# Kernel optimization log

Hardware: AMD Instinct MI355X
Metric: run time of the kernel (lower is better)

## Reference

```python
import jax, jax.numpy as jnp
import numpy as np

ALPHA, BETA, GAMMA = 1.0, 0.5, 0.3
EPS = 1e-08


def setup_inputs() -> dict:
    key = jax.random.key(0)
    k1, k2, k3, k4, k5 = jax.random.split(key, 5)
    B, C, F = 32, 256, 2048
    return {
        "mag_hat": jax.random.normal(k1, (B, C, F), dtype=jnp.float32),
        "phase_hat": jax.random.normal(k2, (B, C, F), dtype=jnp.float32),
        "mag_target": jax.random.normal(k3, (B, C, F), dtype=jnp.float32),
        "phase_target": jax.random.normal(k4, (B, C, F), dtype=jnp.float32),
        "pci_target": jax.random.uniform(k5, (B, C, C), dtype=jnp.float32),
    }


def _pci(phase):
    # phase: (B, C, F). Naive form is mean_f cos/sin(phi_i - phi_j) over a
    # (B,C,C,F) broadcast; rewrite with cos(a-b)=ca*cb+sa*sb and
    # sin(a-b)=sa*cb-ca*sb as two batched GEMMs on (C,F) matrices.
    c = jnp.cos(phase)
    s = jnp.sin(phase)
    inv_f = 1.0 / phase.shape[-1]
    real = (jnp.einsum('bif,bjf->bij', c, c) + jnp.einsum('bif,bjf->bij', s, s)) * inv_f
    imag = (jnp.einsum('bif,bjf->bij', s, c) - jnp.einsum('bif,bjf->bij', c, s)) * inv_f
    return jnp.sqrt(real * real + imag * imag + EPS)


def reference(mag_hat, phase_hat, mag_target, phase_target, pci_target):
    mag_loss = jnp.mean((mag_hat - mag_target) ** 2)
    phase_loss = jnp.mean(1.0 - jnp.cos(phase_hat - phase_target))
    pci_hat = _pci(phase_hat)
    coh_loss = jnp.mean((pci_hat - pci_target) ** 2)
    total = ALPHA * mag_loss + BETA * phase_loss + GAMMA * coh_loss
    return (total, mag_loss, phase_loss, coh_loss)
```

## Files before the change

kernel.cpp:

```cpp
#include <hip/hip_runtime.h>
#include <hip/hip_bf16.h>

#define ALPHA_ 1.0f
#define BETA_  0.5f
#define GAMMA_ 0.3f
#define EPS_   1e-8f

typedef unsigned short u16;
typedef unsigned int u32;

constexpr int B_ = 32, C_ = 256, F_ = 2048;
constexpr int NTOT = B_ * C_ * F_;
constexpr int NCC  = B_ * C_ * C_;
constexpr int NPOS = 10;
constexpr int KSPL = 4;
constexpr int NBLK = B_ * NPOS * KSPL;
constexpr int NRED = B_ * NPOS * 64 * 64;

__constant__ int TI_[NPOS] = {0, 1, 2, 3, 0, 0, 0, 1, 1, 2};
__constant__ int TJ_[NPOS] = {0, 1, 2, 3, 1, 2, 3, 2, 3, 3};

typedef __bf16 bf16x8 __attribute__((ext_vector_type(8)));
typedef float  f32x4  __attribute__((ext_vector_type(4)));

__device__ __forceinline__ u32 f2bf(float x) {
    unsigned u = __float_as_uint(x);
    u += 0x7fffu + ((u >> 16) & 1u);
    return (u >> 16);
}

__device__ __forceinline__ void ew_body(
    float4 p0, float4 p1, float4 q0, float4 q1,
    float4 a0, float4 a1, float4 b0, float4 b1,
    float& msum, float& psum)
{
    float pv[8] = {p0.x, p0.y, p0.z, p0.w, p1.x, p1.y, p1.z, p1.w};
    float qv[8] = {q0.x, q0.y, q0.z, q0.w, q1.x, q1.y, q1.z, q1.w};
    float av[8] = {a0.x, a0.y, a0.z, a0.w, a1.x, a1.y, a1.z, a1.w};
    float bv[8] = {b0.x, b0.y, b0.z, b0.w, b1.x, b1.y, b1.z, b1.w};
    #pragma unroll
    for (int j = 0; j < 8; j++) {
        float dm = av[j] - bv[j];
        msum += dm * dm;
        psum += 1.f - __cosf(pv[j] - qv[j]);
    }
}

__global__ void __launch_bounds__(256, 4)
ew_kernel(const float4* __restrict__ mh, const float4* __restrict__ ph,
          const float4* __restrict__ mt, const float4* __restrict__ pt,
          float* __restrict__ accum)
{
    __shared__ float sm[4], sp[4];
    const int tid = blockIdx.x * 256 + threadIdx.x;
    constexpr int STR = 1024 * 256;
    float msum = 0.f, psum = 0.f;

    float4 P0[8], P1[8], Q0[8], Q1[8], A0[8], A1[8], B0[8], B1[8];

#define EWLOAD(i) { int g2 = 2 * (tid + (i) * STR);            \
    P0[i] = ph[g2]; P1[i] = ph[g2 + 1];                         \
    Q0[i] = pt[g2]; Q1[i] = pt[g2 + 1];                         \
    A0[i] = mh[g2]; A1[i] = mh[g2 + 1];                         \
    B0[i] = mt[g2]; B1[i] = mt[g2 + 1]; }

    EWLOAD(0);
    #pragma unroll
    for (int i = 0; i < 7; ++i) {
        EWLOAD(i + 1);
        __builtin_amdgcn_sched_barrier(0);
        ew_body(P0[i], P1[i], Q0[i], Q1[i], A0[i], A1[i], B0[i], B1[i], msum, psum);
    }
    ew_body(P0[7], P1[7], Q0[7], Q1[7], A0[7], A1[7], B0[7], B1[7], msum, psum);
#undef EWLOAD

    #pragma unroll
    for (int o = 32; o > 0; o >>= 1) {
        msum += __shfl_down(msum, o, 64);
        psum += __shfl_down(psum, o, 64);
    }
    int lane = threadIdx.x & 63, wv = threadIdx.x >> 6;
    if (lane == 0) { sm[wv] = msum; sp[wv] = psum; }
    __syncthreads();
    if (threadIdx.x == 0) {
        atomicAdd(&accum[0], sm[0] + sm[1] + sm[2] + sm[3]);
        atomicAdd(&accum[1], sp[0] + sp[1] + sp[2] + sp[3]);
    }
}

__device__ __forceinline__ void stage8(float4 a, float4 b, char* base, int pc) {
    float v[8] = {a.x, a.y, a.z, a.w, b.x, b.y, b.z, b.w};
    u32 cu[8], su[8];
    #pragma unroll
    for (int j = 0; j < 8; j++) {
        float s, c;
        __sincosf(v[j], &s, &c);
        cu[j] = f2bf(c);
        su[j] = f2bf(s);
    }
    *(int4*)(base + pc) = make_int4(
        (int)(cu[0] | (cu[1] << 16)), (int)(cu[2] | (cu[3] << 16)),
        (int)(cu[4] | (cu[5] << 16)), (int)(cu[6] | (cu[7] << 16)));
    *(int4*)(base + (pc ^ 128)) = make_int4(
        (int)(su[0] | (su[1] << 16)), (int)(su[2] | (su[3] << 16)),
        (int)(su[4] | (su[5] << 16)), (int)(su[6] | (su[7] << 16)));
}

__global__ void __launch_bounds__(256)
pci_kernel(const float* __restrict__ ph, float* __restrict__ slabs)
{
    __shared__ char lds[32768];
    char* la = lds;
    char* lb = lds + 16384;

    const int bid = blockIdx.x;
    const int l   = (bid & 7) * (NBLK / 8) + (bid >> 3);
    const int h   = l & 3;
    const int t4  = l >> 2;
    const int pos = t4 % NPOS;
    const int y   = t4 / NPOS;
    const int i0 = TI_[pos] * 64, j0 = TJ_[pos] * 64;
    const bool diag = (i0 == j0);
    char* lbp = diag ? la : lb;

    const int t    = threadIdx.x;
    const int lane = t & 63, w = t >> 6;
    const int wrow = (w >> 1) * 32, wcol = (w & 1) * 32;
    const int m = lane & 15, q = lane >> 4;

    const int row0 = t >> 3, oct = t & 7;
    const int row1 = row0 + 32;
    const float* gA0 = ph + ((size_t)(y * 256 + i0 + row0) * 2048 + h * 512 + oct * 8);
    const float* gA1 = ph + ((size_t)(y * 256 + i0 + row1) * 2048 + h * 512 + oct * 8);
    const float* gB0 = ph + ((size_t)(y * 256 + j0 + row0) * 2048 + h * 512 + oct * 8);
    const float* gB1 = ph + ((size_t)(y * 256 + j0 + row1) * 2048 + h * 512 + oct * 8);
    char* dA0 = la + row0 * 256;  const int pc0 = (oct ^ (row0 & 15)) * 16;
    char* dA1 = la + row1 * 256;  const int pc1 = (oct ^ (row1 & 15)) * 16;
    char* dB0 = lb + row0 * 256;
    char* dB1 = lb + row1 * 256;

    f32x4 zero = {0.f, 0.f, 0.f, 0.f};
    f32x4 accR[2][2], accSC[2][2], accCS[2][2];
    #pragma unroll
    for (int a = 0; a < 2; a++)
        #pragma unroll
        for (int c = 0; c < 2; c++) {
            accR[a][c] = zero; accSC[a][c] = zero; accCS[a][c] = zero;
        }

    for (int it = 0; it < 8; ++it) {
        __syncthreads();
        float4 a0 = *(const float4*)gA0, a1 = *(const float4*)(gA0 + 4);
        float4 a2 = *(const float4*)gA1, a3 = *(const float4*)(gA1 + 4);
        float4 b0, b1, b2, b3;
        if (!diag) {
            b0 = *(const float4*)gB0; b1 = *(const float4*)(gB0 + 4);
            b2 = *(const float4*)gB1; b3 = *(const float4*)(gB1 + 4);
        }
        gA0 += 64; gA1 += 64; gB0 += 64; gB1 += 64;
        stage8(a0, a1, dA0, pc0);
        stage8(a2, a3, dA1, pc1);
        if (!diag) {
            stage8(b0, b1, dB0, pc0);
            stage8(b2, b3, dB1, pc1);
        }
        __syncthreads();

        #pragma unroll
        for (int s = 0; s < 2; ++s) {
            bf16x8 fac[2], fas[2], fbc[2], fbs[2];
            #pragma unroll
            for (int a = 0; a < 2; a++) {
                const char* base = la + (wrow + a * 16 + m) * 256;
                int pc = ((4 * s + q) ^ m) * 16;
                fac[a] = *(const bf16x8*)(base + pc);
                fas[a] = *(const bf16x8*)(base + (pc ^ 128));
            }
            #pragma unroll
            for (int c = 0; c < 2; c++) {
                const char* base = lbp + (wcol + c * 16 + m) * 256;
                int pc = ((4 * s + q) ^ m) * 16;
                fbc[c] = *(const bf16x8*)(base + pc);
                fbs[c] = *(const bf16x8*)(base + (pc ^ 128));
            }
            #pragma unroll
            for (int a = 0; a < 2; a++)
                #pragma unroll
                for (int c = 0; c < 2; c++) {
                    accR[a][c]  = __builtin_amdgcn_mfma_f32_16x16x32_bf16(fac[a], fbc[c], accR[a][c], 0, 0, 0);
                    accR[a][c]  = __builtin_amdgcn_mfma_f32_16x16x32_bf16(fas[a], fbs[c], accR[a][c], 0, 0, 0);
                    accSC[a][c] = __builtin_amdgcn_mfma_f32_16x16x32_bf16(fas[a], fbc[c], accSC[a][c], 0, 0, 0);
                    accCS[a][c] = __builtin_amdgcn_mfma_f32_16x16x32_bf16(fac[a], fbs[c], accCS[a][c], 0, 0, 0);
                }
        }
    }

    float* sl = slabs + (size_t)h * ((size_t)NRED * 2)
                      + (size_t)(y * NPOS + pos) * 8192;
    #pragma unroll
    for (int a = 0; a < 2; a++)
        #pragma unroll
        for (int c = 0; c < 2; c++) {
            int ii = wrow + a * 16 + q * 4;
            int jj = wcol + c * 16 + m;
            #pragma unroll
            for (int r = 0; r < 4; r++) {
                int idx = (ii + r) * 64 + jj;
                float2 v = make_float2(accR[a][c][r], accSC[a][c][r] - accCS[a][c][r]);
                *(float2*)(sl + (size_t)idx * 2) = v;
            }
        }
}

__global__ void __launch_bounds__(256)
coh_kernel(const float* __restrict__ slabs, const float* __restrict__ tgt,
           float* __restrict__ accum)
{
    __shared__ float sred[4];
    const int tid  = blockIdx.x * 256 + threadIdx.x;
    const int e0   = tid * 8;
    const int tile = e0 >> 12;
    const int y    = tile / NPOS;
    const int pos  = tile % NPOS;
    const int ii   = (e0 & 4095) >> 6;
    const int jj0  = e0 & 63;
    const int ig   = TI_[pos] * 64 + ii;
    const int jg   = TJ_[pos] * 64 + jj0;
    const bool off = (pos >= 4);
    const float invf = 1.0f / (float)F_;
    const float* ty = tgt + (size_t)y * (C_ * C_);
    const float* tr = ty + ig * C_ + jg;

    float rv[8] = {0.f, 0.f, 0.f, 0.f, 0.f, 0.f, 0.f, 0.f};
    float iv[8] = {0.f, 0.f, 0.f, 0.f, 0.f, 0.f, 0.f, 0.f};
    #pragma unroll
    for (int hh = 0; hh < 4; hh++) {
        const float* s = slabs + (size_t)hh * ((size_t)NRED * 2) + (size_t)e0 * 2;
        float4 v0 = *(const float4*)(s);
        float4 v1 = *(const float4*)(s + 4);
        float4 v2 = *(const float4*)(s + 8);
        float4 v3 = *(const float4*)(s + 12);
        rv[0] += v0.x; iv[0] += v0.y; rv[1] += v0.z; iv[1] += v0.w;
        rv[2] += v1.x; iv[2] += v1.y; rv[3] += v1.z; iv[3] += v1.w;
        rv[4] += v2.x; iv[4] += v2.y; rv[5] += v2.z; iv[5] += v2.w;
        rv[6] += v3.x; iv[6] += v3.y; rv[7] += v3.z; iv[7] += v3.w;
    }

    float coh = 0.f;
    #pragma unroll
    for (int j = 0; j < 8; j++) {
        float re = rv[j] * invf, im = iv[j] * invf;
        float p  = sqrtf(re * re + im * im + EPS_);
        float d  = p - tr[j];
        coh += d * d;
        if (off) { float d2 = p - ty[(jg + j) * C_ + ig]; coh += d2 * d2; }
    }

    #pragma unroll
    for (int o = 32; o > 0; o >>= 1) coh += __shfl_down(coh, o, 64);
    int lane = threadIdx.x & 63, w = threadIdx.x >> 6;
    if (lane == 0) sred[w] = coh;
    __syncthreads();
    if (threadIdx.x == 0)
        atomicAdd(&accum[2], sred[0] + sred[1] + sred[2] + sred[3]);
}

__global__ void fin_kernel(const float* __restrict__ accum, float* __restrict__ out)
{
    if (threadIdx.x == 0) {
        float mag = accum[0] * (1.0f / (float)NTOT);
        float phs = accum[1] * (1.0f / (float)NTOT);
        float coh = accum[2] * (1.0f / (float)NCC);
        out[0] = ALPHA_ * mag + BETA_ * phs + GAMMA_ * coh;
        out[1] = mag;
        out[2] = phs;
        out[3] = coh;
    }
}

extern "C" void kernel_launch(void* const* d_in, const int* in_sizes, int n_in,
                              void* d_out, int out_size, void* d_ws, size_t ws_size,
                              hipStream_t stream)
{
    const float* mh  = (const float*)d_in[0];
    const float* ph  = (const float*)d_in[1];
    const float* mt  = (const float*)d_in[2];
    const float* pt  = (const float*)d_in[3];
    const float* tgt = (const float*)d_in[4];
    float* out = (float*)d_out;

    float* accum = (float*)d_ws;
    float* slabs = (float*)((char*)d_ws + 256);

    hipMemsetAsync(d_ws, 0, 16, stream);

    ew_kernel<<<1024, 256, 0, stream>>>(
        (const float4*)mh, (const float4*)ph, (const float4*)mt, (const float4*)pt,
        accum);

    pci_kernel<<<NBLK, 256, 0, stream>>>(ph, slabs);

    coh_kernel<<<640, 256, 0, stream>>>(slabs, tgt, accum);

    fin_kernel<<<1, 64, 0, stream>>>(accum, out);
}
```

Measured before the change: 308.5 us.

## Spread elementwise reduction atomics over slots and transpose coherence tiles via LDS

The elementwise kernel drops its 8-deep software-pipelined loop and instead launches 8192 blocks, one 8-element chunk per thread. Its per-block atomics are spread across 64 partial slots, which the final kernel sums with a wavefront reduction, so contention on a single address goes away. The coherence kernel now handles one 64x64 tile per block. It stages the magnitudes in padded shared memory so the mirrored off-diagonal target can be read coalesced rather than with strided column accesses. Each block does more work and adds a barrier, and the elementwise kernel loses its explicit latency hiding.

Measured after the change: 299.9 us. 1.03x faster.

```diff
diff --git a/kernel.cpp b/kernel.cpp
--- a/kernel.cpp
+++ b/kernel.cpp
@@ -46,33 +46,20 @@
     }
 }
 
-__global__ void __launch_bounds__(256, 4)
+__global__ void __launch_bounds__(256)
 ew_kernel(const float4* __restrict__ mh, const float4* __restrict__ ph,
           const float4* __restrict__ mt, const float4* __restrict__ pt,
-          float* __restrict__ accum)
+          float* __restrict__ part)
 {
     __shared__ float sm[4], sp[4];
-    const int tid = blockIdx.x * 256 + threadIdx.x;
-    constexpr int STR = 1024 * 256;
+    const int g = blockIdx.x * 256 + threadIdx.x;
+    float4 p0 = ph[2*g], p1 = ph[2*g+1];
+    float4 q0 = pt[2*g], q1 = pt[2*g+1];
+    float4 a0 = mh[2*g], a1 = mh[2*g+1];
+    float4 b0 = mt[2*g], b1 = mt[2*g+1];
+
     float msum = 0.f, psum = 0.f;
-
-    float4 P0[8], P1[8], Q0[8], Q1[8], A0[8], A1[8], B0[8], B1[8];
-
-#define EWLOAD(i) { int g2 = 2 * (tid + (i) * STR);            \
-    P0[i] = ph[g2]; P1[i] = ph[g2 + 1];                         \
-    Q0[i] = pt[g2]; Q1[i] = pt[g2 + 1];                         \
-    A0[i] = mh[g2]; A1[i] = mh[g2 + 1];                         \
-    B0[i] = mt[g2]; B1[i] = mt[g2 + 1]; }
-
-    EWLOAD(0);
-    #pragma unroll
-    for (int i = 0; i < 7; ++i) {
-        EWLOAD(i + 1);
-        __builtin_amdgcn_sched_barrier(0);
-        ew_body(P0[i], P1[i], Q0[i], Q1[i], A0[i], A1[i], B0[i], B1[i], msum, psum);
-    }
-    ew_body(P0[7], P1[7], Q0[7], Q1[7], A0[7], A1[7], B0[7], B1[7], msum, psum);
-#undef EWLOAD
+    ew_body(p0, p1, q0, q1, a0, a1, b0, b1, msum, psum);
 
     #pragma unroll
     for (int o = 32; o > 0; o >>= 1) {
@@ -83,8 +70,9 @@
     if (lane == 0) { sm[wv] = msum; sp[wv] = psum; }
     __syncthreads();
     if (threadIdx.x == 0) {
-        atomicAdd(&accum[0], sm[0] + sm[1] + sm[2] + sm[3]);
-        atomicAdd(&accum[1], sp[0] + sp[1] + sp[2] + sp[3]);
+        int slot = blockIdx.x & 63;
+        atomicAdd(&part[slot],      sm[0] + sm[1] + sm[2] + sm[3]);
+        atomicAdd(&part[64 + slot], sp[0] + sp[1] + sp[2] + sp[3]);
     }
 }
 
@@ -216,60 +204,78 @@
 coh_kernel(const float* __restrict__ slabs, const float* __restrict__ tgt,
            float* __restrict__ accum)
 {
+    __shared__ float pl[64 * 65];
     __shared__ float sred[4];
-    const int tid  = blockIdx.x * 256 + threadIdx.x;
-    const int e0   = tid * 8;
-    const int tile = e0 >> 12;
-    const int y    = tile / NPOS;
-    const int pos  = tile % NPOS;
-    const int ii   = (e0 & 4095) >> 6;
-    const int jj0  = e0 & 63;
-    const int ig   = TI_[pos] * 64 + ii;
-    const int jg   = TJ_[pos] * 64 + jj0;
+    const int blk = blockIdx.x;
+    const int y   = blk / NPOS;
+    const int pos = blk % NPOS;
+    const int t   = threadIdx.x;
     const bool off = (pos >= 4);
     const float invf = 1.0f / (float)F_;
+    const int ib = TI_[pos] * 64, jb = TJ_[pos] * 64;
     const float* ty = tgt + (size_t)y * (C_ * C_);
-    const float* tr = ty + ig * C_ + jg;
-
-    float rv[8] = {0.f, 0.f, 0.f, 0.f, 0.f, 0.f, 0.f, 0.f};
-    float iv[8] = {0.f, 0.f, 0.f, 0.f, 0.f, 0.f, 0.f, 0.f};
-    #pragma unroll
-    for (int hh = 0; hh < 4; hh++) {
-        const float* s = slabs + (size_t)hh * ((size_t)NRED * 2) + (size_t)e0 * 2;
-        float4 v0 = *(const float4*)(s);
-        float4 v1 = *(const float4*)(s + 4);
-        float4 v2 = *(const float4*)(s + 8);
-        float4 v3 = *(const float4*)(s + 12);
-        rv[0] += v0.x; iv[0] += v0.y; rv[1] += v0.z; iv[1] += v0.w;
-        rv[2] += v1.x; iv[2] += v1.y; rv[3] += v1.z; iv[3] += v1.w;
-        rv[4] += v2.x; iv[4] += v2.y; rv[5] += v2.z; iv[5] += v2.w;
-        rv[6] += v3.x; iv[6] += v3.y; rv[7] += v3.z; iv[7] += v3.w;
-    }
+    const size_t sb0 = (size_t)(y * NPOS + pos) * 8192;
 
     float coh = 0.f;
     #pragma unroll
-    for (int j = 0; j < 8; j++) {
-        float re = rv[j] * invf, im = iv[j] * invf;
-        float p  = sqrtf(re * re + im * im + EPS_);
-        float d  = p - tr[j];
-        coh += d * d;
-        if (off) { float d2 = p - ty[(jg + j) * C_ + ig]; coh += d2 * d2; }
+    for (int k = 0; k < 8; ++k) {
+        int e = 2 * t + k * 512;
+        float r0 = 0.f, s0 = 0.f, r1 = 0.f, s1 = 0.f;
+        #pragma unroll
+        for (int hh = 0; hh < 4; ++hh) {
+            float4 v = *(const float4*)(slabs
+                + (size_t)hh * ((size_t)NRED * 2) + sb0 + (size_t)e * 2);
+            r0 += v.x; s0 += v.y; r1 += v.z; s1 += v.w;
+        }
+        float re0 = r0 * invf, im0 = s0 * invf;
+        float re1 = r1 * invf, im1 = s1 * invf;
+        float p0 = sqrtf(re0 * re0 + im0 * im0 + EPS_);
+        float p1 = sqrtf(re1 * re1 + im1 * im1 + EPS_);
+        int ii = e >> 6, jj = e & 63;
+        pl[ii * 65 + jj]     = p0;
+        pl[ii * 65 + jj + 1] = p1;
+        float2 tg = *(const float2*)(ty + (size_t)(ib + ii) * C_ + jb + jj);
+        float d0 = p0 - tg.x, d1 = p1 - tg.y;
+        coh += d0 * d0 + d1 * d1;
+    }
+    __syncthreads();
+
+    if (off) {
+        #pragma unroll
+        for (int k = 0; k < 8; ++k) {
+            int e = 2 * t + k * 512;
+            int ii = e >> 6, jj = e & 63;
+            float p0 = pl[jj * 65 + ii];
+            float p1 = pl[(jj + 1) * 65 + ii];
+            float2 tg = *(const float2*)(ty + (size_t)(jb + ii) * C_ + ib + jj);
+            float d0 = p0 - tg.x, d1 = p1 - tg.y;
+            coh += d0 * d0 + d1 * d1;
+        }
     }
 
     #pragma unroll
     for (int o = 32; o > 0; o >>= 1) coh += __shfl_down(coh, o, 64);
-    int lane = threadIdx.x & 63, w = threadIdx.x >> 6;
+    int lane = t & 63, w = t >> 6;
     if (lane == 0) sred[w] = coh;
     __syncthreads();
-    if (threadIdx.x == 0)
+    if (t == 0)
         atomicAdd(&accum[2], sred[0] + sred[1] + sred[2] + sred[3]);
 }
 
-__global__ void fin_kernel(const float* __restrict__ accum, float* __restrict__ out)
-{
-    if (threadIdx.x == 0) {
-        float mag = accum[0] * (1.0f / (float)NTOT);
-        float phs = accum[1] * (1.0f / (float)NTOT);
+__global__ void fin_kernel(const float* __restrict__ accum,
+                           const float* __restrict__ part,
+                           float* __restrict__ out)
+{
+    int t = threadIdx.x;
+    float m = part[t], p = part[64 + t];
+    #pragma unroll
+    for (int o = 32; o > 0; o >>= 1) {
+        m += __shfl_down(m, o, 64);
+        p += __shfl_down(p, o, 64);
+    }
+    if (t == 0) {
+        float mag = m * (1.0f / (float)NTOT);
+        float phs = p * (1.0f / (float)NTOT);
         float coh = accum[2] * (1.0f / (float)NCC);
         out[0] = ALPHA_ * mag + BETA_ * phs + GAMMA_ * coh;
         out[1] = mag;
@@ -290,17 +296,18 @@
     float* out = (float*)d_out;
 
     float* accum = (float*)d_ws;
-    float* slabs = (float*)((char*)d_ws + 256);
-
-    hipMemsetAsync(d_ws, 0, 16, stream);
-
-    ew_kernel<<<1024, 256, 0, stream>>>(
+    float* part  = (float*)((char*)d_ws + 256);
+    float* slabs = (float*)((char*)d_ws + 1024);
+
+    hipMemsetAsync(d_ws, 0, 1024, stream);
+
+    ew_kernel<<<8192, 256, 0, stream>>>(
         (const float4*)mh, (const float4*)ph, (const float4*)mt, (const float4*)pt,
-        accum);
+        part);
 
     pci_kernel<<<NBLK, 256, 0, stream>>>(ph, slabs);
 
-    coh_kernel<<<640, 256, 0, stream>>>(slabs, tgt, accum);
-
-    fin_kernel<<<1, 64, 0, stream>>>(accum, out);
-}
+    coh_kernel<<<320, 256, 0, stream>>>(slabs, tgt, accum);
+
+    fin_kernel<<<1, 64, 0, stream>>>(accum, part, out);
+}
```
